# Optimization experiments

Measured on AMD Instinct MI355X. Metric: run time of the kernel, lower is better.

The kernel has to match this reference:

```python
import jax, jax.numpy as jnp
import numpy as np

B, S, F, K = 32, 4096, 512, 25


def setup_inputs() -> dict:
    key = jax.random.key(0)
    kx, kw = jax.random.split(key)
    x = jax.random.normal(kx, (B, S, F), dtype=jnp.float32)
    # Linear(in=K, out=1, bias=False) weight, flattened to [K]; w[l] multiplies window offset l.
    # (Original inits to zero; use random weights for a meaningful correctness baseline.)
    w = jax.random.normal(kw, (K,), dtype=jnp.float32) / K
    return {"x": x, "w": w}


def reference(x, w):
    # x: [B, S, F]; w: [K]
    b, s, f = x.shape
    k = w.shape[0]
    # Replicate first timestep K-1 times (causal left padding with edge value).
    front = jnp.repeat(x[:, :1, :], k - 1, axis=1)          # [B, K-1, F]
    padded = jnp.concatenate([front, x], axis=1)            # [B, S+K-1, F]
    # out[b, s, f] = sum_l w[l] * padded[b, s+l, f]  == valid cross-correlation.
    # Fused sliding-window dot product via conv1d; shared kernel across all B*F series.
    xr = padded.transpose(0, 2, 1).reshape(b * f, s + k - 1, 1)  # [B*F, S+K-1, 1]
    kern = w.reshape(k, 1, 1)                                    # [K, in=1, out=1]
    out = jax.lax.conv_general_dilated(
        xr, kern, window_strides=(1,), padding='VALID',
        dimension_numbers=('NWC', 'WIO', 'NWC'))                 # [B*F, S, 1]
    return out.reshape(b, f, s).transpose(0, 2, 1)               # [B, S, F]
```

## Files before the change

### kernel.cpp

```cpp
#include <hip/hip_runtime.h>

#define B_   32
#define S_   4096
#define F_   512
#define K_   25
#define F4_  (F_ / 4)
#define SEG  100
#define NSEG ((S_ + SEG - 1) / SEG)

__global__ __launch_bounds__(256, 2)
void adapt_smoothing_kernel(const float* __restrict__ x,
                            const float* __restrict__ w,
                            float* __restrict__ out) {
    const int tid  = blockIdx.x * blockDim.x + threadIdx.x;
    const int f4   = tid & (F4_ - 1);
    const int rest = tid >> 7;
    if (rest >= B_ * NSEG) return;
    const int seg = rest % NSEG;
    const int b   = rest / NSEG;
    const int s0  = seg * SEG;

    float wt[K_];
#pragma unroll
    for (int l = 0; l < K_; ++l) wt[l] = w[l];

    const float4* __restrict__ xcol = (const float4*)(x + (size_t)b * S_ * F_) + f4;
    float4* __restrict__       ocol = (float4*)(out + (size_t)b * S_ * F_) + f4;

    float4 win[K_];
#pragma unroll
    for (int j = 1; j < K_; ++j) {
        int s = s0 - K_ + j;
        s = s < 0 ? 0 : s;
        win[j] = xcol[(size_t)s * F4_];
    }

    for (int i0 = 0; i0 < SEG; i0 += K_) {
#pragma unroll
        for (int u = 0; u < K_; ++u) {
            const int s  = s0 + i0 + u;
            const int sl = s < S_ ? s : (S_ - 1);
            win[u] = xcol[(size_t)sl * F4_];

            float4 acc;
            acc.x = acc.y = acc.z = acc.w = 0.0f;
#pragma unroll
            for (int l = 0; l < K_; ++l) {
                const float4 v = win[(u + 1 + l) % K_];
                const float  c = wt[l];
                acc.x += c * v.x;
                acc.y += c * v.y;
                acc.z += c * v.z;
                acc.w += c * v.w;
            }
            if (s < S_) ocol[(size_t)s * F4_] = acc;
        }
    }
}

extern "C" void kernel_launch(void* const* d_in, const int* in_sizes, int n_in,
                              void* d_out, int out_size, void* d_ws, size_t ws_size,
                              hipStream_t stream) {
    const float* x = (const float*)d_in[0];
    const float* w = (const float*)d_in[1];
    float* out     = (float*)d_out;

    const int total_threads = B_ * NSEG * F4_;
    const int block = 256;
    const int grid  = (total_threads + block - 1) / block;
    adapt_smoothing_kernel<<<grid, block, 0, stream>>>(x, w, out);
}
```

Baseline: 461.4 us.

## Switch to scatter-style rolling accumulators with prefetch and nontemporal stores

Restructures the sliding-window convolution so each input row is loaded once and scattered into a ring of 25 float4 accumulators. This replaces the gather over a 25-entry input window, and the finished output is streamed out with nontemporal stores. The next row is prefetched one step ahead and weights are forced into scalar registers via readfirstlane. Block size drops to 64 threads with different launch bounds, which changes occupancy and register pressure.

```diff
diff --git a/kernel.cpp b/kernel.cpp
--- a/kernel.cpp
+++ b/kernel.cpp
@@ -8,7 +8,9 @@
 #define SEG  100
 #define NSEG ((S_ + SEG - 1) / SEG)
 
-__global__ __launch_bounds__(256, 2)
+typedef float floatx4 __attribute__((ext_vector_type(4)));
+
+__global__ __launch_bounds__(64, 3)
 void adapt_smoothing_kernel(const float* __restrict__ x,
                             const float* __restrict__ w,
                             float* __restrict__ out) {
@@ -22,38 +24,53 @@
 
     float wt[K_];
 #pragma unroll
-    for (int l = 0; l < K_; ++l) wt[l] = w[l];
+    for (int l = 0; l < K_; ++l)
+        wt[l] = __int_as_float(__builtin_amdgcn_readfirstlane(__float_as_int(w[l])));
 
     const float4* __restrict__ xcol = (const float4*)(x + (size_t)b * S_ * F_) + f4;
-    float4* __restrict__       ocol = (float4*)(out + (size_t)b * S_ * F_) + f4;
+    float4*                    ocol = (float4*)(out + (size_t)b * S_ * F_) + f4;
 
-    float4 win[K_];
+    float4 acc[K_];
 #pragma unroll
-    for (int j = 1; j < K_; ++j) {
-        int s = s0 - K_ + j;
-        s = s < 0 ? 0 : s;
-        win[j] = xcol[(size_t)s * F4_];
+    for (int m = 0; m < K_; ++m) acc[m] = make_float4(0.f, 0.f, 0.f, 0.f);
+
+#pragma unroll
+    for (int j = 0; j < K_ - 1; ++j) {
+        int t = s0 - (K_ - 1) + j;
+        t = t < 0 ? 0 : t;
+        const float4 v = xcol[(size_t)t * F4_];
+#pragma unroll
+        for (int m = 0; m <= j; ++m) {
+            const float c = wt[j - m];
+            acc[m].x += c * v.x; acc[m].y += c * v.y;
+            acc[m].z += c * v.z; acc[m].w += c * v.w;
+        }
     }
 
+    float4 v = xcol[(size_t)s0 * F4_];
+#pragma unroll 1
     for (int i0 = 0; i0 < SEG; i0 += K_) {
 #pragma unroll
         for (int u = 0; u < K_; ++u) {
             const int s  = s0 + i0 + u;
-            const int sl = s < S_ ? s : (S_ - 1);
-            win[u] = xcol[(size_t)sl * F4_];
-
-            float4 acc;
-            acc.x = acc.y = acc.z = acc.w = 0.0f;
+            const int sn = (s + 1) < S_ ? (s + 1) : (S_ - 1);
+            const float4 vn = xcol[(size_t)sn * F4_];
 #pragma unroll
-            for (int l = 0; l < K_; ++l) {
-                const float4 v = win[(u + 1 + l) % K_];
-                const float  c = wt[l];
-                acc.x += c * v.x;
-                acc.y += c * v.y;
-                acc.z += c * v.z;
-                acc.w += c * v.w;
+            for (int d = 0; d < K_; ++d) {
+                const float c = wt[K_ - 1 - d];
+                float4& a = acc[(u + d) % K_];
+                if (d == K_ - 1) {
+                    a.x = c * v.x; a.y = c * v.y;
+                    a.z = c * v.z; a.w = c * v.w;
+                } else {
+                    a.x += c * v.x; a.y += c * v.y;
+                    a.z += c * v.z; a.w += c * v.w;
+                }
             }
-            if (s < S_) ocol[(size_t)s * F4_] = acc;
+            if (s < S_)
+                __builtin_nontemporal_store(*(const floatx4*)&acc[u],
+                                            (floatx4*)&ocol[(size_t)s * F4_]);
+            v = vn;
         }
     }
 }
@@ -66,7 +83,7 @@
     float* out     = (float*)d_out;
 
     const int total_threads = B_ * NSEG * F4_;
-    const int block = 256;
+    const int block = 64;
     const int grid  = (total_threads + block - 1) / block;
     adapt_smoothing_kernel<<<grid, block, 0, stream>>>(x, w, out);
 }
```

Measured after the change: 606.7 us. +31.5%, slower.
